# Optimization experiments

Measured on AMD Instinct MI355X. Metric: run time of the kernel, lower is better.

## Reference

```python
import jax, jax.numpy as jnp
import numpy as np

N, F_IN, D, R, E = 50000, 128, 96, 2, 800000


def setup_inputs() -> dict:
    key = jax.random.key(0)
    ks = jax.random.split(key, 8)
    sc = lambda k, shape: jax.random.normal(k, shape, jnp.float32) * 0.05
    return {
        "x": jax.random.normal(ks[0], (N, F_IN), jnp.float32),
        "edge_index": jax.random.randint(ks[1], (2, E), 0, N),
        "edge_attr": jax.random.uniform(ks[2], (E, R), dtype=jnp.float32),
        # nn.Linear(F_IN, D)
        "Wf": sc(ks[3], (D, F_IN)),
        "bf": jnp.zeros((D,), jnp.float32),
        # RGCNConv: per-relation weights, root weight, bias
        "W": sc(ks[4], (R, D, D)),
        "root": sc(ks[5], (D, D)),
        "bias": jnp.zeros((D,), jnp.float32),
    }


def _rgcn_conv(h, src, dst, etype, W, root, bias):
    # PyG RGCNConv (no bases/blocks, aggr='mean'):
    #   out = x @ root + bias + sum_r mean_{edges of type r}(x[src]) @ W[r]
    msg = h[src]  # [E, D] gather
    out = h @ root + bias
    for r in range(R):
        w = (etype == r).astype(h.dtype)[:, None]  # [E, 1] relation mask
        s = jax.ops.segment_sum(msg * w, dst, num_segments=N)   # [N, D] scatter-add
        cnt = jax.ops.segment_sum(w, dst, num_segments=N)       # [N, 1]
        agg = s / jnp.maximum(cnt, 1.0)                          # mean, safe for deg 0
        out = out + agg @ W[r]
    return out


def reference(x, edge_index, edge_attr, Wf, bf, W, root, bias):
    src, dst = edge_index[0], edge_index[1]
    etype = jnp.argmax(edge_attr, axis=1)  # [E]
    h = jax.nn.relu(x @ Wf.T + bf)
    for _ in range(3):
        h = jax.nn.relu(_rgcn_conv(h, src, dst, etype, W, root, bias))
    return h
```

## Files before the change

### kernel.cpp

```cpp
#include <hip/hip_runtime.h>

#define DN 96
#define FIN 128
#define NB 8

typedef unsigned int uint_t;
typedef unsigned short ushort_t;

typedef __attribute__((ext_vector_type(8))) short short8v;
typedef __attribute__((ext_vector_type(4))) float f32x4;

#define MFMA16 __builtin_amdgcn_mfma_f32_16x16x32_bf16

__device__ __forceinline__ ushort_t f2bf(float f) {
    uint_t u = __float_as_uint(f);
    uint_t r = (u + 0x7FFFu + ((u >> 16) & 1u)) >> 16;
    return (ushort_t)r;
}
__device__ __forceinline__ float bf2f(ushort_t h) { return __uint_as_float(((uint_t)h) << 16); }
__device__ __forceinline__ float bf_lo(uint_t u) { return __uint_as_float(u << 16); }
__device__ __forceinline__ float bf_hi(uint_t u) { return __uint_as_float(u & 0xFFFF0000u); }


__global__ void hist_kernel(const int* __restrict__ ei, const float* __restrict__ ea,
                            int* __restrict__ cnt, uint2* __restrict__ kd, int E, int N) {
    int e = blockIdx.x * 256 + threadIdx.x;
    if (e >= E) return;
    int src = ei[e];
    int dst = ei[E + e];
    int r = (ea[2 * e + 1] > ea[2 * e]) ? 1 : 0;
    kd[e] = make_uint2((uint_t)dst | ((uint_t)r << 16), (uint_t)src);
    atomicAdd(&cnt[r * N + dst], 1);
}

__global__ void offsets_kernel(const int* __restrict__ cnt, int* __restrict__ total,
                               int* __restrict__ rowstart, int* __restrict__ fillptr,
                               int nbins) {
    __shared__ int sd[256];
    __shared__ int sbase;
    int t = threadIdx.x;
    int b = blockIdx.x * 256 + t;
    int v = (b < nbins) ? cnt[b] : 0;
    sd[t] = v;
    __syncthreads();
    for (int off = 1; off < 256; off <<= 1) {
        int add = (t >= off) ? sd[t - off] : 0;
        __syncthreads();
        sd[t] += add;
        __syncthreads();
    }
    if (t == 255) sbase = atomicAdd(total, sd[255]);
    __syncthreads();
    if (b < nbins) {
        int s = sbase + sd[t] - v;
        rowstart[b] = s;
        fillptr[b] = s;
    }
}


__global__ __launch_bounds__(256) void fill_part(const uint2* __restrict__ kd,
                            int* __restrict__ fillptr, int* __restrict__ srcs,
                            int E, int N, int PS) {
    int p = blockIdx.x & 7;
    int c = blockIdx.x >> 3;
    int base = c * 2048 + threadIdx.x;
#pragma unroll
    for (int i = 0; i < 8; i++) {
        int e = base + i * 256;
        if (e < E) {
            uint2 v = kd[e];
            int dst = v.x & 0xFFFF;
            if (dst / PS == p) {
                int r = (v.x >> 16) & 1;
                int pos = atomicAdd(&fillptr[r * N + dst], 1);
                srcs[pos] = (int)v.y;
            }
        }
    }
}


__global__ void pack_w(const float* __restrict__ root, const float* __restrict__ W,
                       ushort_t* __restrict__ Bph, ushort_t* __restrict__ Bpl) {
    int l = threadIdx.x;
    int fid = blockIdx.x;
    int ct = fid / 3, ks = fid % 3;
    int mat = ct / 6, cw = ct % 6;
    const float* M = (mat == 0) ? root : (W + (size_t)(mat - 1) * DN * DN);
    int k0 = 32 * ks + (l >> 4) * 8;
    int col = 16 * cw + (l & 15);
#pragma unroll
    for (int j = 0; j < 8; j++) {
        float v = M[(size_t)(k0 + j) * DN + col];
        ushort_t h = f2bf(v);
        size_t idx = ((size_t)fid * 64 + l) * 8 + j;
        Bph[idx] = h;
        Bpl[idx] = f2bf(v - bf2f(h));
    }
}

__global__ void pack_wf(const float* __restrict__ Wf, ushort_t* __restrict__ Wfh,
                        ushort_t* __restrict__ Wfl) {
    int l = threadIdx.x;
    int fid = blockIdx.x;
    int ct = fid >> 2, ks = fid & 3;
    int k0 = 32 * ks + (l >> 4) * 8;
    int col = 16 * ct + (l & 15);
#pragma unroll
    for (int j = 0; j < 8; j++) {
        float v = Wf[(size_t)col * FIN + k0 + j];
        ushort_t h = f2bf(v);
        size_t idx = ((size_t)fid * 64 + l) * 8 + j;
        Wfh[idx] = h;
        Wfl[idx] = f2bf(v - bf2f(h));
    }
}


__device__ __forceinline__ void cvt8(float4 x, float4 y, short8v& hi, short8v& lo) {
    union { short8v v; ushort_t u[8]; } H, L;
    float f[8] = {x.x, x.y, x.z, x.w, y.x, y.y, y.z, y.w};
#pragma unroll
    for (int j = 0; j < 8; j++) {
        ushort_t h = f2bf(f[j]);
        H.u[j] = h;
        L.u[j] = f2bf(f[j] - bf2f(h));
    }
    hi = H.v; lo = L.v;
}


__global__ __launch_bounds__(64) void lin_mfma(const float* __restrict__ x,
                             const ushort_t* __restrict__ Wfh, const ushort_t* __restrict__ Wfl,
                             const float* __restrict__ bf, float* __restrict__ h, int N) {
    int l = threadIdx.x;
    int n0 = blockIdx.x * 16;
    int row = n0 + (l & 15);
    if (row >= N) row = N - 1;
    const float* xrow = x + (size_t)row * FIN + ((l >> 4) * 8);

    short8v ah[4], al[4];
#pragma unroll
    for (int ks = 0; ks < 4; ks++) {
        float4 xa = *(const float4*)(xrow + 32 * ks);
        float4 xb = *(const float4*)(xrow + 32 * ks + 4);
        cvt8(xa, xb, ah[ks], al[ks]);
    }

    for (int ct = 0; ct < 6; ct++) {
        f32x4 ahh = {0.f, 0.f, 0.f, 0.f};
        f32x4 ahl = {0.f, 0.f, 0.f, 0.f};
        f32x4 alh = {0.f, 0.f, 0.f, 0.f};
#pragma unroll
        for (int ks = 0; ks < 4; ks++) {
            const size_t base = ((size_t)(ct * 4 + ks) * 64 + l) * 8;
            short8v bh = *(const short8v*)(Wfh + base);
            short8v bl = *(const short8v*)(Wfl + base);
            ahh = MFMA16(ah[ks], bh, ahh, 0, 0, 0);
            ahl = MFMA16(ah[ks], bl, ahl, 0, 0, 0);
            alh = MFMA16(al[ks], bh, alh, 0, 0, 0);
        }
        f32x4 acc = ahh + ahl + alh;
        int col = ct * 16 + (l & 15);
        int mb = n0 + ((l >> 4) << 2);
        float bv = bf[col];
#pragma unroll
        for (int r = 0; r < 4; r++) {
            int m = mb + r;
            if (m < N) {
                float v = acc[r] + bv;
                h[(size_t)m * DN + col] = v > 0.f ? v : 0.f;
            }
        }
    }
}


__global__ __launch_bounds__(64) void gemm_mfma(float* hb,
                              const ushort_t* __restrict__ Bph, const ushort_t* __restrict__ Bpl,
                              ushort_t* __restrict__ g0, ushort_t* __restrict__ g1,
                              const float* __restrict__ bias, int N) {
    int l = threadIdx.x;
    int n0 = blockIdx.x * 16;
    int row = n0 + (l & 15);
    if (row >= N) row = N - 1;
    const float* hrow = hb + (size_t)row * DN + ((l >> 4) * 8);

    short8v ah[3], al[3];
#pragma unroll
    for (int ks = 0; ks < 3; ks++) {
        float4 xa = *(const float4*)(hrow + 32 * ks);
        float4 xb = *(const float4*)(hrow + 32 * ks + 4);
        cvt8(xa, xb, ah[ks], al[ks]);
    }

    for (int ct = 0; ct < 18; ct++) {
        f32x4 ahh = {0.f, 0.f, 0.f, 0.f};
        f32x4 ahl = {0.f, 0.f, 0.f, 0.f};
        f32x4 alh = {0.f, 0.f, 0.f, 0.f};
#pragma unroll
        for (int ks = 0; ks < 3; ks++) {
            const size_t base = ((size_t)(ct * 3 + ks) * 64 + l) * 8;
            short8v bh = *(const short8v*)(Bph + base);
            short8v bl = *(const short8v*)(Bpl + base);
            ahh = MFMA16(ah[ks], bh, ahh, 0, 0, 0);
            ahl = MFMA16(ah[ks], bl, ahl, 0, 0, 0);
            alh = MFMA16(al[ks], bh, alh, 0, 0, 0);
        }
        f32x4 acc = ahh + ahl + alh;

        int mat = ct / 6;
        int col = (ct % 6) * 16 + (l & 15);
        int mb = n0 + ((l >> 4) << 2);
        if (mat == 0) {
            float bv = bias[col];
#pragma unroll
            for (int r = 0; r < 4; r++) {
                int m = mb + r;
                if (m < N) hb[(size_t)m * DN + col] = acc[r] + bv;
            }
        } else {
            ushort_t* g = (mat == 1) ? g0 : g1;
#pragma unroll
            for (int r = 0; r < 4; r++) {
                int m = mb + r;
                if (m < N) g[(size_t)m * DN + col] = f2bf(acc[r]);
            }
        }
    }
}


__global__ __launch_bounds__(256) void agg_kernel(float* hb, const uint_t* __restrict__ g0,
                           const uint_t* __restrict__ g1, const int* __restrict__ rowstart,
                           const int* __restrict__ cnt, const int* __restrict__ srcs, int N) {
    int t = threadIdx.x;
    int hw = t >> 5;
    int m = t & 31;
    int n = blockIdx.x * NB + hw;
    if (n >= N || m >= 24) return;

    size_t off = (size_t)n * DN + 4 * m;
    float4 hv = *(const float4*)(hb + off);

    int b0 = rowstart[n], c0 = cnt[n];
    int b1 = rowstart[N + n], c1 = cnt[N + n];

    float acc0 = 0.f, acc1 = 0.f, acc2 = 0.f, acc3 = 0.f;
#pragma unroll
    for (int r = 0; r < 2; r++) {
        const uint_t* g = r ? g1 : g0;
        int base = r ? b1 : b0;
        int c = r ? c1 : c0;
        const int* sp = srcs + base;
        float s0 = 0.f, s1 = 0.f, s2 = 0.f, s3 = 0.f;
        int e = 0;
        for (; e + 4 <= c; e += 4) {
            int i0 = sp[e], i1 = sp[e + 1], i2 = sp[e + 2], i3 = sp[e + 3];
            uint2 v0 = *(const uint2*)(g + (size_t)i0 * 48 + 2 * m);
            uint2 v1 = *(const uint2*)(g + (size_t)i1 * 48 + 2 * m);
            uint2 v2 = *(const uint2*)(g + (size_t)i2 * 48 + 2 * m);
            uint2 v3 = *(const uint2*)(g + (size_t)i3 * 48 + 2 * m);
            s0 += (bf_lo(v0.x) + bf_lo(v1.x)) + (bf_lo(v2.x) + bf_lo(v3.x));
            s1 += (bf_hi(v0.x) + bf_hi(v1.x)) + (bf_hi(v2.x) + bf_hi(v3.x));
            s2 += (bf_lo(v0.y) + bf_lo(v1.y)) + (bf_lo(v2.y) + bf_lo(v3.y));
            s3 += (bf_hi(v0.y) + bf_hi(v1.y)) + (bf_hi(v2.y) + bf_hi(v3.y));
        }
        for (; e < c; e++) {
            uint2 v = *(const uint2*)(g + (size_t)sp[e] * 48 + 2 * m);
            s0 += bf_lo(v.x);
            s1 += bf_hi(v.x);
            s2 += bf_lo(v.y);
            s3 += bf_hi(v.y);
        }
        float inv = (c > 0) ? 1.f / (float)c : 0.f;
        acc0 += s0 * inv;
        acc1 += s1 * inv;
        acc2 += s2 * inv;
        acc3 += s3 * inv;
    }
    float4 o;
    o.x = hv.x + acc0; o.x = o.x > 0.f ? o.x : 0.f;
    o.y = hv.y + acc1; o.y = o.y > 0.f ? o.y : 0.f;
    o.z = hv.z + acc2; o.z = o.z > 0.f ? o.z : 0.f;
    o.w = hv.w + acc3; o.w = o.w > 0.f ? o.w : 0.f;
    *(float4*)(hb + off) = o;
}

extern "C" void kernel_launch(void* const* d_in, const int* in_sizes, int n_in,
                              void* d_out, int out_size, void* d_ws, size_t ws_size,
                              hipStream_t stream) {
    const float* x    = (const float*)d_in[0];
    const int*   ei   = (const int*)d_in[1];
    const float* ea   = (const float*)d_in[2];
    const float* Wf   = (const float*)d_in[3];
    const float* bf   = (const float*)d_in[4];
    const float* W    = (const float*)d_in[5];
    const float* root = (const float*)d_in[6];
    const float* bias = (const float*)d_in[7];
    float* out = (float*)d_out;

    int N = in_sizes[0] / FIN;
    int E = in_sizes[1] / 2;
    int nbins = 2 * N;
    int PS = (N + 7) / 8;

    int* cnt      = (int*)d_ws;
    int* total    = cnt + nbins;
    int* rowstart = cnt + nbins + 4;
    int* fillptr  = rowstart + nbins;
    int* srcs     = fillptr + nbins;
    uint2* kd     = (uint2*)(srcs + E);
    ushort_t* Bph = (ushort_t*)(kd + E);
    ushort_t* Bpl = Bph + 54 * 64 * 8;
    ushort_t* Wfh = Bpl + 54 * 64 * 8;
    ushort_t* Wfl = Wfh + 24 * 64 * 8;
    ushort_t* g0  = Wfl + 24 * 64 * 8;
    ushort_t* g1  = g0 + (size_t)N * DN;

    hipMemsetAsync(cnt, 0, (size_t)(nbins + 1) * sizeof(int), stream);

    hist_kernel<<<(E + 255) / 256, 256, 0, stream>>>(ei, ea, cnt, kd, E, N);
    offsets_kernel<<<(nbins + 255) / 256, 256, 0, stream>>>(cnt, total, rowstart, fillptr, nbins);
    int nchunk = (E + 2047) / 2048;
    fill_part<<<nchunk * 8, 256, 0, stream>>>(kd, fillptr, srcs, E, N, PS);
    pack_w<<<54, 64, 0, stream>>>(root, W, Bph, Bpl);
    pack_wf<<<24, 64, 0, stream>>>(Wf, Wfh, Wfl);

    int gblk = (N + 15) / 16;
    lin_mfma<<<gblk, 64, 0, stream>>>(x, Wfh, Wfl, bf, out, N);

    int nblk = (N + NB - 1) / NB;
    for (int lyr = 0; lyr < 3; lyr++) {
        gemm_mfma<<<gblk, 64, 0, stream>>>(out, Bph, Bpl, g0, g1, bias, N);
        agg_kernel<<<nblk, 256, 0, stream>>>(out, (const uint_t*)g0, (const uint_t*)g1,
                                             rowstart, cnt, srcs, N);
    }
}
```

Measured before the change: 319.6 us.

## Fuse aggregation with next layer's GEMM via shared-memory staging and ping-pong buffers

Replaces the separate linear, per-layer GEMM and aggregation kernels with one templated layer kernel. Each launch aggregates neighbour messages for 16 nodes, applies the ReLU, stages the result in shared memory and immediately runs the next layer's root/relation GEMM on it, so the intermediate h round-trip through global memory and several launches go away. The first launch fuses the input linear layer with the first GEMM, and the two weight-pack kernels are merged into one. Gather lanes now read 6 bf16 values each with 16 lanes per node. The cost is ping-pong workspace buffers, a block-level sync, and GEMM work split across 4 waves that each handle fewer column tiles.

```diff
diff --git a/kernel.cpp b/kernel.cpp
--- a/kernel.cpp
+++ b/kernel.cpp
@@ -2,7 +2,6 @@
 
 #define DN 96
 #define FIN 128
-#define NB 8
 
 typedef unsigned int uint_t;
 typedef unsigned short ushort_t;
@@ -11,6 +10,8 @@
 typedef __attribute__((ext_vector_type(4))) float f32x4;
 
 #define MFMA16 __builtin_amdgcn_mfma_f32_16x16x32_bf16
+
+struct __align__(4) U3 { uint_t x, y, z; };
 
 __device__ __forceinline__ ushort_t f2bf(float f) {
     uint_t u = __float_as_uint(f);
@@ -81,39 +82,40 @@
 }
 
 
-__global__ void pack_w(const float* __restrict__ root, const float* __restrict__ W,
-                       ushort_t* __restrict__ Bph, ushort_t* __restrict__ Bpl) {
+__global__ void pack_all(const float* __restrict__ root, const float* __restrict__ W,
+                         const float* __restrict__ Wf,
+                         ushort_t* __restrict__ Bph, ushort_t* __restrict__ Bpl,
+                         ushort_t* __restrict__ Wfh, ushort_t* __restrict__ Wfl) {
     int l = threadIdx.x;
-    int fid = blockIdx.x;
-    int ct = fid / 3, ks = fid % 3;
-    int mat = ct / 6, cw = ct % 6;
-    const float* M = (mat == 0) ? root : (W + (size_t)(mat - 1) * DN * DN);
-    int k0 = 32 * ks + (l >> 4) * 8;
-    int col = 16 * cw + (l & 15);
-#pragma unroll
-    for (int j = 0; j < 8; j++) {
-        float v = M[(size_t)(k0 + j) * DN + col];
-        ushort_t h = f2bf(v);
-        size_t idx = ((size_t)fid * 64 + l) * 8 + j;
-        Bph[idx] = h;
-        Bpl[idx] = f2bf(v - bf2f(h));
-    }
-}
-
-__global__ void pack_wf(const float* __restrict__ Wf, ushort_t* __restrict__ Wfh,
-                        ushort_t* __restrict__ Wfl) {
-    int l = threadIdx.x;
-    int fid = blockIdx.x;
-    int ct = fid >> 2, ks = fid & 3;
-    int k0 = 32 * ks + (l >> 4) * 8;
-    int col = 16 * ct + (l & 15);
-#pragma unroll
-    for (int j = 0; j < 8; j++) {
-        float v = Wf[(size_t)col * FIN + k0 + j];
-        ushort_t h = f2bf(v);
-        size_t idx = ((size_t)fid * 64 + l) * 8 + j;
-        Wfh[idx] = h;
-        Wfl[idx] = f2bf(v - bf2f(h));
+    int bid = blockIdx.x;
+    if (bid < 54) {
+        int fid = bid;
+        int ct = fid / 3, ks = fid % 3;
+        int mat = ct / 6, cw = ct % 6;
+        const float* M = (mat == 0) ? root : (W + (size_t)(mat - 1) * DN * DN);
+        int k0 = 32 * ks + (l >> 4) * 8;
+        int col = 16 * cw + (l & 15);
+#pragma unroll
+        for (int j = 0; j < 8; j++) {
+            float v = M[(size_t)(k0 + j) * DN + col];
+            ushort_t h = f2bf(v);
+            size_t idx = ((size_t)fid * 64 + l) * 8 + j;
+            Bph[idx] = h;
+            Bpl[idx] = f2bf(v - bf2f(h));
+        }
+    } else {
+        int fid = bid - 54;
+        int ct = fid >> 2, ks = fid & 3;
+        int k0 = 32 * ks + (l >> 4) * 8;
+        int col = 16 * ct + (l & 15);
+#pragma unroll
+        for (int j = 0; j < 8; j++) {
+            float v = Wf[(size_t)col * FIN + k0 + j];
+            ushort_t h = f2bf(v);
+            size_t idx = ((size_t)fid * 64 + l) * 8 + j;
+            Wfh[idx] = h;
+            Wfl[idx] = f2bf(v - bf2f(h));
+        }
     }
 }
 
@@ -131,161 +133,176 @@
 }
 
 
-__global__ __launch_bounds__(64) void lin_mfma(const float* __restrict__ x,
-                             const ushort_t* __restrict__ Wfh, const ushort_t* __restrict__ Wfl,
-                             const float* __restrict__ bf, float* __restrict__ h, int N) {
-    int l = threadIdx.x;
-    int n0 = blockIdx.x * 16;
-    int row = n0 + (l & 15);
-    if (row >= N) row = N - 1;
-    const float* xrow = x + (size_t)row * FIN + ((l >> 4) * 8);
-
-    short8v ah[4], al[4];
-#pragma unroll
-    for (int ks = 0; ks < 4; ks++) {
-        float4 xa = *(const float4*)(xrow + 32 * ks);
-        float4 xb = *(const float4*)(xrow + 32 * ks + 4);
-        cvt8(xa, xb, ah[ks], al[ks]);
-    }
-
-    for (int ct = 0; ct < 6; ct++) {
-        f32x4 ahh = {0.f, 0.f, 0.f, 0.f};
-        f32x4 ahl = {0.f, 0.f, 0.f, 0.f};
-        f32x4 alh = {0.f, 0.f, 0.f, 0.f};
+template <int MODE>
+__global__ __launch_bounds__(256) void layer_kernel(
+    const float* __restrict__ xin,
+    const float* __restrict__ hrootIn,
+    const uint_t* __restrict__ g0In, const uint_t* __restrict__ g1In,
+    const int* __restrict__ rowstart, const int* __restrict__ cnt,
+    const int* __restrict__ srcs,
+    const ushort_t* __restrict__ WfH, const ushort_t* __restrict__ WfL,
+    const ushort_t* __restrict__ Bph, const ushort_t* __restrict__ Bpl,
+    const float* __restrict__ bfv, const float* __restrict__ bias,
+    float* __restrict__ hrootOut, ushort_t* __restrict__ g0Out, ushort_t* __restrict__ g1Out,
+    float* __restrict__ dout, int N)
+{
+    constexpr int NW = (MODE == 0) ? 4 : 1;
+    __shared__ float sout[NW][16][100];
+    int t = threadIdx.x;
+    int l = t & 63;
+    int w = t >> 6;
+
+    if constexpr (MODE == 0) {
+        int slab = blockIdx.x * 64 + w * 16;
+        int row = slab + (l & 15);
+        if (row >= N) row = N - 1;
+        const float* xrow = xin + (size_t)row * FIN + ((l >> 4) * 8);
+        short8v ah[4], al[4];
 #pragma unroll
         for (int ks = 0; ks < 4; ks++) {
-            const size_t base = ((size_t)(ct * 4 + ks) * 64 + l) * 8;
-            short8v bh = *(const short8v*)(Wfh + base);
-            short8v bl = *(const short8v*)(Wfl + base);
-            ahh = MFMA16(ah[ks], bh, ahh, 0, 0, 0);
-            ahl = MFMA16(ah[ks], bl, ahl, 0, 0, 0);
-            alh = MFMA16(al[ks], bh, alh, 0, 0, 0);
-        }
-        f32x4 acc = ahh + ahl + alh;
-        int col = ct * 16 + (l & 15);
-        int mb = n0 + ((l >> 4) << 2);
-        float bv = bf[col];
-#pragma unroll
-        for (int r = 0; r < 4; r++) {
-            int m = mb + r;
-            if (m < N) {
+            float4 xa = *(const float4*)(xrow + 32 * ks);
+            float4 xb = *(const float4*)(xrow + 32 * ks + 4);
+            cvt8(xa, xb, ah[ks], al[ks]);
+        }
+#pragma unroll
+        for (int ct = 0; ct < 6; ct++) {
+            f32x4 hh = {0.f,0.f,0.f,0.f}, hl_ = {0.f,0.f,0.f,0.f}, lh = {0.f,0.f,0.f,0.f};
+#pragma unroll
+            for (int ks = 0; ks < 4; ks++) {
+                size_t base = ((size_t)(ct * 4 + ks) * 64 + l) * 8;
+                short8v bh = *(const short8v*)(WfH + base);
+                short8v bl = *(const short8v*)(WfL + base);
+                hh  = MFMA16(ah[ks], bh, hh, 0, 0, 0);
+                hl_ = MFMA16(ah[ks], bl, hl_, 0, 0, 0);
+                lh  = MFMA16(al[ks], bh, lh, 0, 0, 0);
+            }
+            f32x4 acc = hh + hl_ + lh;
+            int col = ct * 16 + (l & 15);
+            float bv = bfv[col];
+            int lr0 = (l >> 4) * 4;
+#pragma unroll
+            for (int r = 0; r < 4; r++) {
                 float v = acc[r] + bv;
-                h[(size_t)m * DN + col] = v > 0.f ? v : 0.f;
-            }
-        }
-    }
-}
-
-
-__global__ __launch_bounds__(64) void gemm_mfma(float* hb,
-                              const ushort_t* __restrict__ Bph, const ushort_t* __restrict__ Bpl,
-                              ushort_t* __restrict__ g0, ushort_t* __restrict__ g1,
-                              const float* __restrict__ bias, int N) {
-    int l = threadIdx.x;
-    int n0 = blockIdx.x * 16;
-    int row = n0 + (l & 15);
-    if (row >= N) row = N - 1;
-    const float* hrow = hb + (size_t)row * DN + ((l >> 4) * 8);
-
-    short8v ah[3], al[3];
-#pragma unroll
-    for (int ks = 0; ks < 3; ks++) {
-        float4 xa = *(const float4*)(hrow + 32 * ks);
-        float4 xb = *(const float4*)(hrow + 32 * ks + 4);
-        cvt8(xa, xb, ah[ks], al[ks]);
-    }
-
-    for (int ct = 0; ct < 18; ct++) {
-        f32x4 ahh = {0.f, 0.f, 0.f, 0.f};
-        f32x4 ahl = {0.f, 0.f, 0.f, 0.f};
-        f32x4 alh = {0.f, 0.f, 0.f, 0.f};
+                sout[w][lr0 + r][col] = v > 0.f ? v : 0.f;
+            }
+        }
+    } else {
+        int grp = t >> 4;
+        int j = t & 15;
+        int n = blockIdx.x * 16 + grp;
+        bool valid = n < N;
+        int nc = valid ? n : N - 1;
+        float a0=0.f,a1=0.f,a2=0.f,a3=0.f,a4=0.f,a5=0.f;
+#pragma unroll
+        for (int r = 0; r < 2; r++) {
+            int c    = valid ? cnt[r * N + nc] : 0;
+            int base = valid ? rowstart[r * N + nc] : 0;
+            const uint_t* g = r ? g1In : g0In;
+            const int* sp = srcs + base;
+            float s0=0.f,s1=0.f,s2=0.f,s3=0.f,s4=0.f,s5=0.f;
+            int e = 0;
+            for (; e + 4 <= c; e += 4) {
+                int i0 = sp[e], i1 = sp[e+1], i2 = sp[e+2], i3 = sp[e+3];
+                U3 v0 = *(const U3*)(g + (size_t)i0 * 48 + 3 * j);
+                U3 v1 = *(const U3*)(g + (size_t)i1 * 48 + 3 * j);
+                U3 v2 = *(const U3*)(g + (size_t)i2 * 48 + 3 * j);
+                U3 v3 = *(const U3*)(g + (size_t)i3 * 48 + 3 * j);
+                s0 += (bf_lo(v0.x) + bf_lo(v1.x)) + (bf_lo(v2.x) + bf_lo(v3.x));
+                s1 += (bf_hi(v0.x) + bf_hi(v1.x)) + (bf_hi(v2.x) + bf_hi(v3.x));
+                s2 += (bf_lo(v0.y) + bf_lo(v1.y)) + (bf_lo(v2.y) + bf_lo(v3.y));
+                s3 += (bf_hi(v0.y) + bf_hi(v1.y)) + (bf_hi(v2.y) + bf_hi(v3.y));
+                s4 += (bf_lo(v0.z) + bf_lo(v1.z)) + (bf_lo(v2.z) + bf_lo(v3.z));
+                s5 += (bf_hi(v0.z) + bf_hi(v1.z)) + (bf_hi(v2.z) + bf_hi(v3.z));
+            }
+            for (; e < c; e++) {
+                U3 v = *(const U3*)(g + (size_t)sp[e] * 48 + 3 * j);
+                s0 += bf_lo(v.x); s1 += bf_hi(v.x);
+                s2 += bf_lo(v.y); s3 += bf_hi(v.y);
+                s4 += bf_lo(v.z); s5 += bf_hi(v.z);
+            }
+            float inv = (c > 0) ? 1.f / (float)c : 0.f;
+            a0 += s0 * inv; a1 += s1 * inv; a2 += s2 * inv;
+            a3 += s3 * inv; a4 += s4 * inv; a5 += s5 * inv;
+        }
+        const float* hr = hrootIn + (size_t)nc * DN + 6 * j;
+        float2 p0 = *(const float2*)hr;
+        float2 p1 = *(const float2*)(hr + 2);
+        float2 p2 = *(const float2*)(hr + 4);
+        float o0 = fmaxf(p0.x + a0, 0.f);
+        float o1 = fmaxf(p0.y + a1, 0.f);
+        float o2 = fmaxf(p1.x + a2, 0.f);
+        float o3 = fmaxf(p1.y + a3, 0.f);
+        float o4 = fmaxf(p2.x + a4, 0.f);
+        float o5 = fmaxf(p2.y + a5, 0.f);
+        if constexpr (MODE == 1) {
+            float* dr = &sout[0][grp][6 * j];
+            dr[0]=o0; dr[1]=o1; dr[2]=o2; dr[3]=o3; dr[4]=o4; dr[5]=o5;
+        } else {
+            if (valid) {
+                float* dr = dout + (size_t)n * DN + 6 * j;
+                *(float2*)(dr)     = make_float2(o0, o1);
+                *(float2*)(dr + 2) = make_float2(o2, o3);
+                *(float2*)(dr + 4) = make_float2(o4, o5);
+            }
+        }
+    }
+
+    if constexpr (MODE == 2) return;
+    __syncthreads();
+
+    {
+        const float* srow;
+        int mbase;
+        if constexpr (MODE == 0) {
+            srow = &sout[w][l & 15][0];
+            mbase = blockIdx.x * 64 + w * 16 + ((l >> 4) << 2);
+        } else {
+            srow = &sout[0][l & 15][0];
+            mbase = blockIdx.x * 16 + ((l >> 4) << 2);
+        }
+        int k0 = (l >> 4) * 8;
+        short8v ah[3], al[3];
 #pragma unroll
         for (int ks = 0; ks < 3; ks++) {
-            const size_t base = ((size_t)(ct * 3 + ks) * 64 + l) * 8;
-            short8v bh = *(const short8v*)(Bph + base);
-            short8v bl = *(const short8v*)(Bpl + base);
-            ahh = MFMA16(ah[ks], bh, ahh, 0, 0, 0);
-            ahl = MFMA16(ah[ks], bl, ahl, 0, 0, 0);
-            alh = MFMA16(al[ks], bh, alh, 0, 0, 0);
-        }
-        f32x4 acc = ahh + ahl + alh;
-
-        int mat = ct / 6;
-        int col = (ct % 6) * 16 + (l & 15);
-        int mb = n0 + ((l >> 4) << 2);
-        if (mat == 0) {
-            float bv = bias[col];
-#pragma unroll
-            for (int r = 0; r < 4; r++) {
-                int m = mb + r;
-                if (m < N) hb[(size_t)m * DN + col] = acc[r] + bv;
-            }
-        } else {
-            ushort_t* g = (mat == 1) ? g0 : g1;
-#pragma unroll
-            for (int r = 0; r < 4; r++) {
-                int m = mb + r;
-                if (m < N) g[(size_t)m * DN + col] = f2bf(acc[r]);
-            }
-        }
-    }
-}
-
-
-__global__ __launch_bounds__(256) void agg_kernel(float* hb, const uint_t* __restrict__ g0,
-                           const uint_t* __restrict__ g1, const int* __restrict__ rowstart,
-                           const int* __restrict__ cnt, const int* __restrict__ srcs, int N) {
-    int t = threadIdx.x;
-    int hw = t >> 5;
-    int m = t & 31;
-    int n = blockIdx.x * NB + hw;
-    if (n >= N || m >= 24) return;
-
-    size_t off = (size_t)n * DN + 4 * m;
-    float4 hv = *(const float4*)(hb + off);
-
-    int b0 = rowstart[n], c0 = cnt[n];
-    int b1 = rowstart[N + n], c1 = cnt[N + n];
-
-    float acc0 = 0.f, acc1 = 0.f, acc2 = 0.f, acc3 = 0.f;
-#pragma unroll
-    for (int r = 0; r < 2; r++) {
-        const uint_t* g = r ? g1 : g0;
-        int base = r ? b1 : b0;
-        int c = r ? c1 : c0;
-        const int* sp = srcs + base;
-        float s0 = 0.f, s1 = 0.f, s2 = 0.f, s3 = 0.f;
-        int e = 0;
-        for (; e + 4 <= c; e += 4) {
-            int i0 = sp[e], i1 = sp[e + 1], i2 = sp[e + 2], i3 = sp[e + 3];
-            uint2 v0 = *(const uint2*)(g + (size_t)i0 * 48 + 2 * m);
-            uint2 v1 = *(const uint2*)(g + (size_t)i1 * 48 + 2 * m);
-            uint2 v2 = *(const uint2*)(g + (size_t)i2 * 48 + 2 * m);
-            uint2 v3 = *(const uint2*)(g + (size_t)i3 * 48 + 2 * m);
-            s0 += (bf_lo(v0.x) + bf_lo(v1.x)) + (bf_lo(v2.x) + bf_lo(v3.x));
-            s1 += (bf_hi(v0.x) + bf_hi(v1.x)) + (bf_hi(v2.x) + bf_hi(v3.x));
-            s2 += (bf_lo(v0.y) + bf_lo(v1.y)) + (bf_lo(v2.y) + bf_lo(v3.y));
-            s3 += (bf_hi(v0.y) + bf_hi(v1.y)) + (bf_hi(v2.y) + bf_hi(v3.y));
-        }
-        for (; e < c; e++) {
-            uint2 v = *(const uint2*)(g + (size_t)sp[e] * 48 + 2 * m);
-            s0 += bf_lo(v.x);
-            s1 += bf_hi(v.x);
-            s2 += bf_lo(v.y);
-            s3 += bf_hi(v.y);
-        }
-        float inv = (c > 0) ? 1.f / (float)c : 0.f;
-        acc0 += s0 * inv;
-        acc1 += s1 * inv;
-        acc2 += s2 * inv;
-        acc3 += s3 * inv;
-    }
-    float4 o;
-    o.x = hv.x + acc0; o.x = o.x > 0.f ? o.x : 0.f;
-    o.y = hv.y + acc1; o.y = o.y > 0.f ? o.y : 0.f;
-    o.z = hv.z + acc2; o.z = o.z > 0.f ? o.z : 0.f;
-    o.w = hv.w + acc3; o.w = o.w > 0.f ? o.w : 0.f;
-    *(float4*)(hb + off) = o;
+            float4 xa = *(const float4*)(srow + k0 + 32 * ks);
+            float4 xb = *(const float4*)(srow + k0 + 32 * ks + 4);
+            cvt8(xa, xb, ah[ks], al[ks]);
+        }
+        int ctS, ctC;
+        if constexpr (MODE == 0) { ctS = 0; ctC = 18; }
+        else { ctS = (w < 2) ? 5 * w : 10 + 4 * (w - 2); ctC = (w < 2) ? 5 : 4; }
+        for (int ci = 0; ci < ctC; ci++) {
+            int ct = ctS + ci;
+            f32x4 hh = {0.f,0.f,0.f,0.f}, hl_ = {0.f,0.f,0.f,0.f}, lh = {0.f,0.f,0.f,0.f};
+#pragma unroll
+            for (int ks = 0; ks < 3; ks++) {
+                size_t base = ((size_t)(ct * 3 + ks) * 64 + l) * 8;
+                short8v bh = *(const short8v*)(Bph + base);
+                short8v bl = *(const short8v*)(Bpl + base);
+                hh  = MFMA16(ah[ks], bh, hh, 0, 0, 0);
+                hl_ = MFMA16(ah[ks], bl, hl_, 0, 0, 0);
+                lh  = MFMA16(al[ks], bh, lh, 0, 0, 0);
+            }
+            f32x4 acc = hh + hl_ + lh;
+            int mat = ct / 6;
+            int col = (ct % 6) * 16 + (l & 15);
+            if (mat == 0) {
+                float bv = bias[col];
+#pragma unroll
+                for (int r = 0; r < 4; r++) {
+                    int m = mbase + r;
+                    if (m < N) hrootOut[(size_t)m * DN + col] = acc[r] + bv;
+                }
+            } else {
+                ushort_t* g = (mat == 1) ? g0Out : g1Out;
+#pragma unroll
+                for (int r = 0; r < 4; r++) {
+                    int m = mbase + r;
+                    if (m < N) g[(size_t)m * DN + col] = f2bf(acc[r]);
+                }
+            }
+        }
+    }
 }
 
 extern "C" void kernel_launch(void* const* d_in, const int* in_sizes, int n_in,
@@ -313,11 +330,15 @@
     int* srcs     = fillptr + nbins;
     uint2* kd     = (uint2*)(srcs + E);
     ushort_t* Bph = (ushort_t*)(kd + E);
-    ushort_t* Bpl = Bph + 54 * 64 * 8;
-    ushort_t* Wfh = Bpl + 54 * 64 * 8;
-    ushort_t* Wfl = Wfh + 24 * 64 * 8;
-    ushort_t* g0  = Wfl + 24 * 64 * 8;
-    ushort_t* g1  = g0 + (size_t)N * DN;
+    ushort_t* Bpl = Bph + 54 * 512;
+    ushort_t* Wfh = Bpl + 54 * 512;
+    ushort_t* Wfl = Wfh + 24 * 512;
+    float* hrootA = (float*)(Wfl + 24 * 512);
+    ushort_t* g0A = (ushort_t*)(hrootA + (size_t)N * DN);
+    ushort_t* g1A = g0A + (size_t)N * DN;
+    float* hrootB = (float*)(g1A + (size_t)N * DN);
+    ushort_t* g0B = (ushort_t*)(hrootB + (size_t)N * DN);
+    ushort_t* g1B = g0B + (size_t)N * DN;
 
     hipMemsetAsync(cnt, 0, (size_t)(nbins + 1) * sizeof(int), stream);
 
@@ -325,16 +346,21 @@
     offsets_kernel<<<(nbins + 255) / 256, 256, 0, stream>>>(cnt, total, rowstart, fillptr, nbins);
     int nchunk = (E + 2047) / 2048;
     fill_part<<<nchunk * 8, 256, 0, stream>>>(kd, fillptr, srcs, E, N, PS);
-    pack_w<<<54, 64, 0, stream>>>(root, W, Bph, Bpl);
-    pack_wf<<<24, 64, 0, stream>>>(Wf, Wfh, Wfl);
-
-    int gblk = (N + 15) / 16;
-    lin_mfma<<<gblk, 64, 0, stream>>>(x, Wfh, Wfl, bf, out, N);
-
-    int nblk = (N + NB - 1) / NB;
-    for (int lyr = 0; lyr < 3; lyr++) {
-        gemm_mfma<<<gblk, 64, 0, stream>>>(out, Bph, Bpl, g0, g1, bias, N);
-        agg_kernel<<<nblk, 256, 0, stream>>>(out, (const uint_t*)g0, (const uint_t*)g1,
-                                             rowstart, cnt, srcs, N);
-    }
-}
+    pack_all<<<78, 64, 0, stream>>>(root, W, Wf, Bph, Bpl, Wfh, Wfl);
+
+    int blk64 = (N + 63) / 64;
+    int blk16 = (N + 15) / 16;
+
+    layer_kernel<0><<<blk64, 256, 0, stream>>>(
+        x, nullptr, nullptr, nullptr, rowstart, cnt, srcs,
+        Wfh, Wfl, Bph, Bpl, bf, bias, hrootA, g0A, g1A, nullptr, N);
+    layer_kernel<1><<<blk16, 256, 0, stream>>>(
+        nullptr, hrootA, (const uint_t*)g0A, (const uint_t*)g1A, rowstart, cnt, srcs,
+        nullptr, nullptr, Bph, Bpl, nullptr, bias, hrootB, g0B, g1B, nullptr, N);
+    layer_kernel<1><<<blk16, 256, 0, stream>>>(
+        nullptr, hrootB, (const uint_t*)g0B, (const uint_t*)g1B, rowstart, cnt, srcs,
+        nullptr, nullptr, Bph, Bpl, nullptr, bias, hrootA, g0A, g1A, nullptr, N);
+    layer_kernel<2><<<blk16, 256, 0, stream>>>(
+        nullptr, hrootA, (const uint_t*)g0A, (const uint_t*)g1A, rowstart, cnt, srcs,
+        nullptr, nullptr, nullptr, nullptr, nullptr, nullptr, nullptr, nullptr, nullptr, out, N);
+}
```

After: 294.3 us. 1.09x faster.
